# Performance work log

Hardware: AMD Instinct MI355X
Metric: run time of the kernel (lower is better)

Reference implementation:

```python
import jax, jax.numpy as jnp
import numpy as np

B, N1, N2, D = 4096, 16, 32, 30   # node batch, 1st-hop nbrs, 2nd-hop nbrs, nodeDataLen
H, HD = 6, 5                       # heads, head_dim (embed_dim = size_out*heads = 30)
LH = 64                            # linear_hidden
NEG_SLOPE = 0.02


def setup_inputs() -> dict:
    key = jax.random.key(0)
    ks = jax.random.split(key, 20)
    def w(k, shape, std=0.2):
        return jax.random.normal(k, shape, dtype=jnp.float32) * std
    return {
        "x2": jax.random.normal(ks[0], (B, N1, N2, D), dtype=jnp.float32),
        "self_feat": jax.random.normal(ks[1], (B, D), dtype=jnp.float32),
        # second-hop GraphLayer params (size_in=30 -> embed 30)
        "lin_w2": w(ks[2], (D, D)), "lin_b2": jnp.zeros((D,), jnp.float32),
        "in_w2": w(ks[3], (3 * D, D), 0.1), "in_b2": jnp.zeros((3 * D,), jnp.float32),
        "out_w2": w(ks[4], (D, D), 0.1), "out_b2": jnp.zeros((D,), jnp.float32),
        # first-hop GraphLayer params
        "lin_w1": w(ks[5], (D, D)), "lin_b1": jnp.zeros((D,), jnp.float32),
        "in_w1": w(ks[6], (3 * D, D), 0.1), "in_b1": jnp.zeros((3 * D,), jnp.float32),
        "out_w1": w(ks[7], (D, D), 0.1), "out_b1": jnp.zeros((D,), jnp.float32),
        # classification MLP
        "cw1": w(ks[8], (LH, D), 0.02), "cb1": jnp.zeros((LH,), jnp.float32),
        "cw2": w(ks[9], (LH, LH), 0.02), "cb2": jnp.zeros((LH,), jnp.float32),
        "cw3": w(ks[10], (2, LH), 0.02), "cb3": jnp.zeros((2,), jnp.float32),
    }


def graph_layer(x, lw, lb, iw, ib, ow, ob):
    """x: [S, D] -> Linear + LeakyReLU(0.02) + MHA(self) + mean over S -> [D].
    Dropout(0.2) is identity in eval mode."""
    S = x.shape[0]
    y = jax.nn.leaky_relu(x @ lw.T + lb, NEG_SLOPE)          # [S, D]
    qkv = y @ iw.T + ib                                       # [S, 3D] packed in_proj
    q, k, v = jnp.split(qkv, 3, axis=-1)
    q = q.reshape(S, H, HD)
    k = k.reshape(S, H, HD)
    v = v.reshape(S, H, HD)
    scores = jnp.einsum('shd,thd->hst', q, k) / np.float32(np.sqrt(HD))
    att = jax.nn.softmax(scores, axis=-1)                     # [H, S, S]
    o = jnp.einsum('hst,thd->shd', att, v).reshape(S, H * HD) # [S, D]
    o = o @ ow.T + ob
    return o.mean(axis=0)                                     # [D]


def reference(x2, self_feat,
              lin_w2, lin_b2, in_w2, in_b2, out_w2, out_b2,
              lin_w1, lin_b1, in_w1, in_b1, out_w1, out_b1,
              cw1, cb1, cw2, cb2, cw3, cb3):
    gl2 = lambda x: graph_layer(x, lin_w2, lin_b2, in_w2, in_b2, out_w2, out_b2)
    h1 = jax.vmap(jax.vmap(gl2))(x2)                          # [B, N1, D] second-hop aggregation
    seq = jnp.concatenate([h1, self_feat[:, None, :]], axis=1)  # [B, N1+1, D] append current node
    gl1 = lambda x: graph_layer(x, lin_w1, lin_b1, in_w1, in_b1, out_w1, out_b1)
    emb = jax.vmap(gl1)(seq)                                  # [B, D]
    h = jax.nn.leaky_relu(emb @ cw1.T + cb1, NEG_SLOPE)
    h = jax.nn.leaky_relu(h @ cw2.T + cb2, NEG_SLOPE)
    logits = h @ cw3.T + cb3                                  # [B, 2]
    # original applies Softmax(dim=0) to the 1-D 2-vector per node == softmax over classes
    return jax.nn.softmax(logits, axis=-1)
```

## Files before the change

kernel.cpp:

```cpp
#include <hip/hip_runtime.h>
#include <math.h>

#define LRELU(v) ((v) > 0.0f ? (v) : 0.02f * (v))

typedef __attribute__((ext_vector_type(8)))  short short8;
typedef __attribute__((ext_vector_type(4)))  float f32x4;
typedef __attribute__((ext_vector_type(16))) float f32x16;
typedef __attribute__((ext_vector_type(2)))  int   int2v;

__device__ inline short f2bf(float f) {
    unsigned u = __builtin_bit_cast(unsigned, f);
    unsigned r = (u + 0x7FFFu + ((u >> 16) & 1u)) >> 16;
    return (short)r;
}
__device__ inline int pack_bf16_trunc(float a, float b) {
    unsigned ua = __builtin_bit_cast(unsigned, a);
    unsigned ub = __builtin_bit_cast(unsigned, b);
    return (int)((ub & 0xFFFF0000u) | (ua >> 16));
}
__device__ inline float bf16s_to_f(unsigned short u) {
    unsigned v = ((unsigned)u) << 16;
    return __builtin_bit_cast(float, v);
}

#define PAIRS 8
#define NP1   2
#define RS5   0.44721359549995793f

__global__ __launch_bounds__(256, 4) void gl2_kernel(
    const float* __restrict__ x2,
    const float* __restrict__ lw, const float* __restrict__ lb,
    const float* __restrict__ iw, const float* __restrict__ ib,
    const float* __restrict__ ow, const float* __restrict__ ob,
    float* __restrict__ h1out)
{
    __shared__ short y_lds[32][40];
    __shared__ short qmf[6][33][8];
    __shared__ short kmf[6][33][8];
    __shared__ float vT[6][5][36];
    __shared__ short att2[6][32][40];
    __shared__ float abar[6][32];
    __shared__ float obar[32];

    const int tid  = threadIdx.x;
    const int lane = tid & 63;
    const int w    = tid >> 6;
    const int l15  = lane & 15;
    const int lq   = lane >> 4;
    const int h5   = lane >> 5;
    const int scol = lane & 31;
    const int rowz = (lane < 32) ? scol : 32;

    for (int i = tid; i < (6 * 33 * 8) / 2; i += 256) {
        ((int*)qmf)[i] = 0; ((int*)kmf)[i] = 0;
    }
    if (tid < 2) obar[30 + tid] = 0.0f;

    const int di = w & 1, si = w >> 1;
    short8 blw; float lbv;
    {
        int d = di * 16 + l15;
        #pragma unroll
        for (int i = 0; i < 8; ++i) {
            int k = lq * 8 + i;
            blw[i] = f2bf((d < 30 && k < 30) ? lw[d * 30 + k] : 0.0f);
        }
        lbv = (d < 30) ? lb[d] : 0.0f;
    }
    const int jtA = (3 * w) >> 1, jtB = (3 * w + 2) >> 1;
    short8 biwA, biwB; float ibvA, ibvB;
    {
        int jA = jtA * 16 + l15, jB = jtB * 16 + l15;
        #pragma unroll
        for (int i = 0; i < 8; ++i) {
            int k = lq * 8 + i;
            biwA[i] = f2bf((jA < 90 && k < 30) ? iw[jA * 30 + k] : 0.0f);
            biwB[i] = f2bf((jB < 90 && k < 30) ? iw[jB * 30 + k] : 0.0f);
        }
        ibvA = (jA < 90) ? ib[jA] : 0.0f;
        ibvB = (jB < 90) ? ib[jB] : 0.0f;
    }
    __syncthreads();

    for (int p = 0; p < PAIRS; ++p) {
        const long pair = (long)blockIdx.x * PAIRS + p;
        const float* xp = x2 + pair * 960;

        {
            short8 af;
            int s = si * 16 + l15;
            #pragma unroll
            for (int i = 0; i < 8; ++i) {
                int k = lq * 8 + i;
                af[i] = f2bf((k < 30) ? xp[s * 30 + k] : 0.0f);
            }
            f32x4 c = {0.0f, 0.0f, 0.0f, 0.0f};
            c = __builtin_amdgcn_mfma_f32_16x16x32_bf16(af, blw, c, 0, 0, 0);
            #pragma unroll
            for (int r = 0; r < 4; ++r) {
                float yv = c[r] + lbv;
                yv = LRELU(yv);
                y_lds[si * 16 + lq * 4 + r][di * 16 + l15] = f2bf(yv);
            }
        }
        __syncthreads();

        {
            short8 a0 = *(const short8*)&y_lds[l15][lq * 8];
            short8 a1 = *(const short8*)&y_lds[16 + l15][lq * 8];
            #pragma unroll
            for (int t = 0; t < 3; ++t) {
                int T = 3 * w + t, jt = T >> 1, si_ = T & 1;
                short8 a = si_ ? a1 : a0;
                short8 b = (jt == jtA) ? biwA : biwB;
                float ibv = (jt == jtA) ? ibvA : ibvB;
                f32x4 c = {0.0f, 0.0f, 0.0f, 0.0f};
                c = __builtin_amdgcn_mfma_f32_16x16x32_bf16(a, b, c, 0, 0, 0);
                int j = jt * 16 + l15;
                int s0 = si_ * 16 + lq * 4;
                if (j < 30) {
                    int h = j / 5, e = j - 5 * h;
                    #pragma unroll
                    for (int r = 0; r < 4; ++r)
                        qmf[h][s0 + r][e] = f2bf(c[r] + ibv);
                } else if (j < 60) {
                    int jj = j - 30; int h = jj / 5, e = jj - 5 * h;
                    #pragma unroll
                    for (int r = 0; r < 4; ++r)
                        kmf[h][s0 + r][e] = f2bf((c[r] + ibv) * RS5);
                } else if (j < 90) {
                    int jj = j - 60; int h = jj / 5, e = jj - 5 * h;
                    #pragma unroll
                    for (int r = 0; r < 4; ++r)
                        vT[h][e][s0 + r] = c[r] + ibv;
                }
            }
        }
        __syncthreads();

        if (w < 3) {
            #pragma unroll
            for (int hh = 0; hh < 2; ++hh) {
                const int h = 2 * w + hh;
                short8 af = *(const short8*)&kmf[h][rowz][0];
                short8 bf = *(const short8*)&qmf[h][rowz][0];
                f32x16 c;
                #pragma unroll
                for (int r = 0; r < 16; ++r) c[r] = 0.0f;
                c = __builtin_amdgcn_mfma_f32_32x32x16_bf16(af, bf, c, 0, 0, 0);
                float m = c[0];
                #pragma unroll
                for (int r = 1; r < 16; ++r) m = fmaxf(m, c[r]);
                m = fmaxf(m, __shfl_xor(m, 32));
                float Z = 0.0f;
                #pragma unroll
                for (int r = 0; r < 16; ++r) { c[r] = __expf(c[r] - m); Z += c[r]; }
                Z += __shfl_xor(Z, 32);
                float rZ = (1.0f / 32.0f) / Z;
                #pragma unroll
                for (int g = 0; g < 4; ++g) {
                    int tb = 8 * g + 4 * h5;
                    int2v wv;
                    wv.x = pack_bf16_trunc(c[4 * g] * rZ, c[4 * g + 1] * rZ);
                    wv.y = pack_bf16_trunc(c[4 * g + 2] * rZ, c[4 * g + 3] * rZ);
                    *(int2v*)&att2[h][scol][tb] = wv;
                }
            }
        }
        __syncthreads();

        if (tid < 192) {
            const int h = tid >> 5, t = tid & 31;
            float sum = 0.0f;
            #pragma unroll
            for (int s = 0; s < 32; ++s)
                sum += bf16s_to_f((unsigned short)att2[h][s][t]);
            abar[h][t] = sum;
        }
        __syncthreads();

        if (tid < 240) {
            const int he = tid >> 3, tq = tid & 7;
            const int h = he / 5, e = he - 5 * h;
            f32x4 av = *(const f32x4*)&abar[h][tq * 4];
            f32x4 vv = *(const f32x4*)&vT[h][e][tq * 4];
            float part = av.x * vv.x + av.y * vv.y + av.z * vv.z + av.w * vv.w;
            part += __shfl_down(part, 4, 8);
            part += __shfl_down(part, 2, 8);
            part += __shfl_down(part, 1, 8);
            if (tq == 0) obar[he] = part;
        }
        __syncthreads();

        if (tid < 240) {
            const int d = tid >> 3, jq = tid & 7;
            f32x4 ov = *(const f32x4*)&obar[jq * 4];
            float part = 0.0f;
            #pragma unroll
            for (int i = 0; i < 4; ++i) {
                int j = jq * 4 + i;
                if (j < 30) part = fmaf(ov[i], ow[d * 30 + j], part);
            }
            part += __shfl_down(part, 4, 8);
            part += __shfl_down(part, 2, 8);
            part += __shfl_down(part, 1, 8);
            if (jq == 0) h1out[pair * 30 + d] = part + ob[d];
        }
    }
}

__global__ __launch_bounds__(256, 4) void gl1_mlp_kernel(
    const float* __restrict__ h1, const float* __restrict__ self_feat,
    const float* __restrict__ lw, const float* __restrict__ lb,
    const float* __restrict__ iw, const float* __restrict__ ib,
    const float* __restrict__ ow, const float* __restrict__ ob,
    const float* __restrict__ cw1, const float* __restrict__ cb1,
    const float* __restrict__ cw2, const float* __restrict__ cb2,
    const float* __restrict__ cw3, const float* __restrict__ cb3,
    float* __restrict__ out)
{
    __shared__ short y_lds[32][40];
    __shared__ short qmf[6][33][8];
    __shared__ short kmf[6][33][8];
    __shared__ float vT[6][5][36];
    __shared__ short att2[6][32][40];
    __shared__ float abar[6][32];
    __shared__ float obar[32];
    __shared__ float embb[32];
    __shared__ float hb1[64];
    __shared__ float hb2[64];
    __shared__ float lg[2];

    const int tid  = threadIdx.x;
    const int lane = tid & 63;
    const int w    = tid >> 6;
    const int l15  = lane & 15;
    const int lq   = lane >> 4;
    const int h5   = lane >> 5;
    const int scol = lane & 31;
    const int rowz = (lane < 32) ? scol : 32;

    for (int i = tid; i < (6 * 33 * 8) / 2; i += 256) {
        ((int*)qmf)[i] = 0; ((int*)kmf)[i] = 0;
    }
    if (tid < 2) obar[30 + tid] = 0.0f;

    const int di = w & 1, si = w >> 1;
    short8 blw; float lbv;
    {
        int d = di * 16 + l15;
        #pragma unroll
        for (int i = 0; i < 8; ++i) {
            int k = lq * 8 + i;
            blw[i] = f2bf((d < 30 && k < 30) ? lw[d * 30 + k] : 0.0f);
        }
        lbv = (d < 30) ? lb[d] : 0.0f;
    }
    const int jtA = (3 * w) >> 1, jtB = (3 * w + 2) >> 1;
    short8 biwA, biwB; float ibvA, ibvB;
    {
        int jA = jtA * 16 + l15, jB = jtB * 16 + l15;
        #pragma unroll
        for (int i = 0; i < 8; ++i) {
            int k = lq * 8 + i;
            biwA[i] = f2bf((jA < 90 && k < 30) ? iw[jA * 30 + k] : 0.0f);
            biwB[i] = f2bf((jB < 90 && k < 30) ? iw[jB * 30 + k] : 0.0f);
        }
        ibvA = (jA < 90) ? ib[jA] : 0.0f;
        ibvB = (jB < 90) ? ib[jB] : 0.0f;
    }
    __syncthreads();

    for (int p = 0; p < NP1; ++p) {
        const long node = (long)blockIdx.x * NP1 + p;
        const float* h1p = h1 + node * 480;
        const float* sfp = self_feat + node * 30;

        {
            short8 af;
            if (si == 0) {
                int s = l15;
                #pragma unroll
                for (int i = 0; i < 8; ++i) {
                    int k = lq * 8 + i;
                    af[i] = f2bf((k < 30) ? h1p[s * 30 + k] : 0.0f);
                }
            } else {
                #pragma unroll
                for (int i = 0; i < 8; ++i) {
                    int k = lq * 8 + i;
                    af[i] = (l15 == 0 && k < 30) ? f2bf(sfp[k]) : (short)0;
                }
            }
            f32x4 c = {0.0f, 0.0f, 0.0f, 0.0f};
            c = __builtin_amdgcn_mfma_f32_16x16x32_bf16(af, blw, c, 0, 0, 0);
            #pragma unroll
            for (int r = 0; r < 4; ++r) {
                float yv = c[r] + lbv;
                yv = LRELU(yv);
                y_lds[si * 16 + lq * 4 + r][di * 16 + l15] = f2bf(yv);
            }
        }
        __syncthreads();

        {
            short8 a0 = *(const short8*)&y_lds[l15][lq * 8];
            short8 a1 = *(const short8*)&y_lds[16 + l15][lq * 8];
            #pragma unroll
            for (int t = 0; t < 3; ++t) {
                int T = 3 * w + t, jt = T >> 1, si_ = T & 1;
                short8 a = si_ ? a1 : a0;
                short8 b = (jt == jtA) ? biwA : biwB;
                float ibv = (jt == jtA) ? ibvA : ibvB;
                f32x4 c = {0.0f, 0.0f, 0.0f, 0.0f};
                c = __builtin_amdgcn_mfma_f32_16x16x32_bf16(a, b, c, 0, 0, 0);
                int j = jt * 16 + l15;
                int s0 = si_ * 16 + lq * 4;
                if (j < 30) {
                    int h = j / 5, e = j - 5 * h;
                    #pragma unroll
                    for (int r = 0; r < 4; ++r)
                        qmf[h][s0 + r][e] = f2bf(c[r] + ibv);
                } else if (j < 60) {
                    int jj = j - 30; int h = jj / 5, e = jj - 5 * h;
                    #pragma unroll
                    for (int r = 0; r < 4; ++r)
                        kmf[h][s0 + r][e] = f2bf((c[r] + ibv) * RS5);
                } else if (j < 90) {
                    int jj = j - 60; int h = jj / 5, e = jj - 5 * h;
                    #pragma unroll
                    for (int r = 0; r < 4; ++r)
                        vT[h][e][s0 + r] = c[r] + ibv;
                }
            }
        }
        __syncthreads();

        if (w < 3) {
            #pragma unroll
            for (int hh = 0; hh < 2; ++hh) {
                const int h = 2 * w + hh;
                short8 af = *(const short8*)&kmf[h][rowz][0];
                short8 bf = *(const short8*)&qmf[h][rowz][0];
                f32x16 c;
                #pragma unroll
                for (int r = 0; r < 16; ++r) c[r] = 0.0f;
                c = __builtin_amdgcn_mfma_f32_32x32x16_bf16(af, bf, c, 0, 0, 0);
                #pragma unroll
                for (int r = 0; r < 16; ++r) {
                    int tr = (r & 3) + 8 * (r >> 2) + 4 * h5;
                    c[r] = (tr < 17) ? c[r] : -1e30f;
                }
                float m = c[0];
                #pragma unroll
                for (int r = 1; r < 16; ++r) m = fmaxf(m, c[r]);
                m = fmaxf(m, __shfl_xor(m, 32));
                float Z = 0.0f;
                #pragma unroll
                for (int r = 0; r < 16; ++r) { c[r] = __expf(c[r] - m); Z += c[r]; }
                Z += __shfl_xor(Z, 32);
                float rZ = (1.0f / 17.0f) / Z;
                #pragma unroll
                for (int g = 0; g < 4; ++g) {
                    int tb = 8 * g + 4 * h5;
                    int2v wv;
                    wv.x = pack_bf16_trunc(c[4 * g] * rZ, c[4 * g + 1] * rZ);
                    wv.y = pack_bf16_trunc(c[4 * g + 2] * rZ, c[4 * g + 3] * rZ);
                    *(int2v*)&att2[h][scol][tb] = wv;
                }
            }
        }
        __syncthreads();

        if (tid < 192) {
            const int h = tid >> 5, t = tid & 31;
            float sum = 0.0f;
            #pragma unroll
            for (int s = 0; s < 17; ++s)
                sum += bf16s_to_f((unsigned short)att2[h][s][t]);
            abar[h][t] = sum;
        }
        __syncthreads();

        if (tid < 240) {
            const int he = tid >> 3, tq = tid & 7;
            const int h = he / 5, e = he - 5 * h;
            f32x4 av = *(const f32x4*)&abar[h][tq * 4];
            f32x4 vv = *(const f32x4*)&vT[h][e][tq * 4];
            float part = av.x * vv.x + av.y * vv.y + av.z * vv.z + av.w * vv.w;
            part += __shfl_down(part, 4, 8);
            part += __shfl_down(part, 2, 8);
            part += __shfl_down(part, 1, 8);
            if (tq == 0) obar[he] = part;
        }
        __syncthreads();

        if (tid < 240) {
            const int d = tid >> 3, jq = tid & 7;
            f32x4 ov = *(const f32x4*)&obar[jq * 4];
            float part = 0.0f;
            #pragma unroll
            for (int i = 0; i < 4; ++i) {
                int j = jq * 4 + i;
                if (j < 30) part = fmaf(ov[i], ow[d * 30 + j], part);
            }
            part += __shfl_down(part, 4, 8);
            part += __shfl_down(part, 2, 8);
            part += __shfl_down(part, 1, 8);
            if (jq == 0) embb[d] = part + ob[d];
        }
        __syncthreads();

        {
            const int o = tid >> 2, kq = tid & 3;
            float part = 0.0f;
            #pragma unroll
            for (int i = 0; i < 8; ++i) {
                int k = kq * 8 + i;
                if (k < 30) part = fmaf(embb[k], cw1[o * 30 + k], part);
            }
            part += __shfl_down(part, 2, 4);
            part += __shfl_down(part, 1, 4);
            if (kq == 0) hb1[o] = LRELU(part + cb1[o]);
        }
        __syncthreads();
        {
            const int o = tid >> 2, kq = tid & 3;
            float part = 0.0f;
            #pragma unroll
            for (int i = 0; i < 16; ++i) {
                int k = kq * 16 + i;
                part = fmaf(hb1[k], cw2[o * 64 + k], part);
            }
            part += __shfl_down(part, 2, 4);
            part += __shfl_down(part, 1, 4);
            if (kq == 0) hb2[o] = LRELU(part + cb2[o]);
        }
        __syncthreads();
        if (tid < 128) {
            const int c = tid >> 6, k = tid & 63;
            float part = hb2[k] * cw3[c * 64 + k];
            part += __shfl_down(part, 32);
            part += __shfl_down(part, 16);
            part += __shfl_down(part, 8);
            part += __shfl_down(part, 4);
            part += __shfl_down(part, 2);
            part += __shfl_down(part, 1);
            if (k == 0) lg[c] = part + cb3[c];
        }
        __syncthreads();
        if (tid < 2) {
            float m = fmaxf(lg[0], lg[1]);
            float e0 = __expf(lg[0] - m), e1 = __expf(lg[1] - m);
            float pr = ((tid == 0) ? e0 : e1) / (e0 + e1);
            out[node * 2 + tid] = pr;
        }
        __syncthreads();
    }
}

extern "C" void kernel_launch(void* const* d_in, const int* in_sizes, int n_in,
                              void* d_out, int out_size, void* d_ws, size_t ws_size,
                              hipStream_t stream)
{
    const float* x2        = (const float*)d_in[0];
    const float* self_feat = (const float*)d_in[1];
    const float* lin_w2 = (const float*)d_in[2];
    const float* lin_b2 = (const float*)d_in[3];
    const float* in_w2  = (const float*)d_in[4];
    const float* in_b2  = (const float*)d_in[5];
    const float* out_w2 = (const float*)d_in[6];
    const float* out_b2 = (const float*)d_in[7];
    const float* lin_w1 = (const float*)d_in[8];
    const float* lin_b1 = (const float*)d_in[9];
    const float* in_w1  = (const float*)d_in[10];
    const float* in_b1  = (const float*)d_in[11];
    const float* out_w1 = (const float*)d_in[12];
    const float* out_b1 = (const float*)d_in[13];
    const float* cw1 = (const float*)d_in[14];
    const float* cb1 = (const float*)d_in[15];
    const float* cw2 = (const float*)d_in[16];
    const float* cb2 = (const float*)d_in[17];
    const float* cw3 = (const float*)d_in[18];
    const float* cb3 = (const float*)d_in[19];
    float* outp = (float*)d_out;

    float* h1 = (float*)d_ws;

    gl2_kernel<<<(4096 * 16) / PAIRS, 256, 0, stream>>>(
        x2, lin_w2, lin_b2, in_w2, in_b2, out_w2, out_b2, h1);

    gl1_mlp_kernel<<<4096 / NP1, 256, 0, stream>>>(
        h1, self_feat, lin_w1, lin_b1, in_w1, in_b1, out_w1, out_b1,
        cw1, cb1, cw2, cb2, cw3, cb3, outp);
}
```

Before: 573.1 us.

## Fuse attention-mean and V product into MFMA, use hardware bf16 pack and exp2

The attention-weighted V reduction is now done with two MFMAs directly from the softmax registers against a bf16 V tile stored in a permuted layout. This removes the att2/abar LDS round trips and two block barriers per pair. The K scale is folded with log2(e) so the softmax can use raw v_exp_f32 and rcp. It also uses v_cvt_pk_bf16_f32 for packing, raises the occupancy hint to 5, and gives gl1 one node per block instead of two. These trade a more complex swizzled layout and reduced-precision reciprocal and exp for fewer LDS passes and syncs.

```diff
diff --git a/kernel.cpp b/kernel.cpp
--- a/kernel.cpp
+++ b/kernel.cpp
@@ -1,45 +1,44 @@
 #include <hip/hip_runtime.h>
 #include <math.h>
 
-#define LRELU(v) ((v) > 0.0f ? (v) : 0.02f * (v))
+#define LRELU(v) fmaxf((v), 0.02f * (v))
 
 typedef __attribute__((ext_vector_type(8)))  short short8;
 typedef __attribute__((ext_vector_type(4)))  float f32x4;
 typedef __attribute__((ext_vector_type(16))) float f32x16;
 typedef __attribute__((ext_vector_type(2)))  int   int2v;
+typedef __attribute__((ext_vector_type(4)))  int   int4v;
 
 __device__ inline short f2bf(float f) {
     unsigned u = __builtin_bit_cast(unsigned, f);
     unsigned r = (u + 0x7FFFu + ((u >> 16) & 1u)) >> 16;
     return (short)r;
 }
-__device__ inline int pack_bf16_trunc(float a, float b) {
-    unsigned ua = __builtin_bit_cast(unsigned, a);
-    unsigned ub = __builtin_bit_cast(unsigned, b);
-    return (int)((ub & 0xFFFF0000u) | (ua >> 16));
+__device__ inline int cvt_pk_bf16(float lo, float hi) {
+    int r;
+    asm("v_cvt_pk_bf16_f32 %0, %1, %2" : "=v"(r) : "v"(lo), "v"(hi));
+    return r;
 }
-__device__ inline float bf16s_to_f(unsigned short u) {
-    unsigned v = ((unsigned)u) << 16;
-    return __builtin_bit_cast(float, v);
+__device__ inline float exp2_asm(float x) {
+    float r;
+    asm("v_exp_f32 %0, %1" : "=v"(r) : "v"(x));
+    return r;
 }
 
 #define PAIRS 8
-#define NP1   2
-#define RS5   0.44721359549995793f
-
-__global__ __launch_bounds__(256, 4) void gl2_kernel(
+#define RS5L  0.6451994329f
+
+__global__ __launch_bounds__(256, 5) void gl2_kernel(
     const float* __restrict__ x2,
     const float* __restrict__ lw, const float* __restrict__ lb,
     const float* __restrict__ iw, const float* __restrict__ ib,
     const float* __restrict__ ow, const float* __restrict__ ob,
     float* __restrict__ h1out)
 {
-    __shared__ short y_lds[32][40];
-    __shared__ short qmf[6][33][8];
-    __shared__ short kmf[6][33][8];
-    __shared__ float vT[6][5][36];
-    __shared__ short att2[6][32][40];
-    __shared__ float abar[6][32];
+    __shared__ __attribute__((aligned(16))) short y_lds[32][40];
+    __shared__ __attribute__((aligned(16))) short qmf[6][33][8];
+    __shared__ __attribute__((aligned(16))) short kmf[6][33][8];
+    __shared__ __attribute__((aligned(16))) short vbf[6][8][40];
     __shared__ float obar[32];
 
     const int tid  = threadIdx.x;
@@ -51,9 +50,8 @@
     const int scol = lane & 31;
     const int rowz = (lane < 32) ? scol : 32;
 
-    for (int i = tid; i < (6 * 33 * 8) / 2; i += 256) {
-        ((int*)qmf)[i] = 0; ((int*)kmf)[i] = 0;
-    }
+    for (int i = tid; i < 792; i += 256) { ((int*)qmf)[i] = 0; ((int*)kmf)[i] = 0; }
+    for (int i = tid; i < 960; i += 256) ((int*)vbf)[i] = 0;
     if (tid < 2) obar[30 + tid] = 0.0f;
 
     const int di = w & 1, si = w >> 1;
@@ -87,21 +85,30 @@
         const float* xp = x2 + pair * 960;
 
         {
-            short8 af;
             int s = si * 16 + l15;
+            const float* xr = xp + s * 30 + lq * 8;
+            float xv[8];
             #pragma unroll
             for (int i = 0; i < 8; ++i) {
                 int k = lq * 8 + i;
-                af[i] = f2bf((k < 30) ? xp[s * 30 + k] : 0.0f);
-            }
+                xv[i] = (k < 30) ? xr[i] : 0.0f;
+            }
+            int4v ai;
+            ai.x = cvt_pk_bf16(xv[0], xv[1]);
+            ai.y = cvt_pk_bf16(xv[2], xv[3]);
+            ai.z = cvt_pk_bf16(xv[4], xv[5]);
+            ai.w = cvt_pk_bf16(xv[6], xv[7]);
+            short8 af = __builtin_bit_cast(short8, ai);
             f32x4 c = {0.0f, 0.0f, 0.0f, 0.0f};
             c = __builtin_amdgcn_mfma_f32_16x16x32_bf16(af, blw, c, 0, 0, 0);
-            #pragma unroll
-            for (int r = 0; r < 4; ++r) {
-                float yv = c[r] + lbv;
-                yv = LRELU(yv);
-                y_lds[si * 16 + lq * 4 + r][di * 16 + l15] = f2bf(yv);
-            }
+            float y0 = LRELU(c[0] + lbv), y1 = LRELU(c[1] + lbv);
+            float y2 = LRELU(c[2] + lbv), y3 = LRELU(c[3] + lbv);
+            int p01 = cvt_pk_bf16(y0, y1), p23 = cvt_pk_bf16(y2, y3);
+            int row = si * 16 + lq * 4, col = di * 16 + l15;
+            y_lds[row + 0][col] = (short)p01;
+            y_lds[row + 1][col] = (short)(p01 >> 16);
+            y_lds[row + 2][col] = (short)p23;
+            y_lds[row + 3][col] = (short)(p23 >> 16);
         }
         __syncthreads();
 
@@ -120,19 +127,28 @@
                 int s0 = si_ * 16 + lq * 4;
                 if (j < 30) {
                     int h = j / 5, e = j - 5 * h;
-                    #pragma unroll
-                    for (int r = 0; r < 4; ++r)
-                        qmf[h][s0 + r][e] = f2bf(c[r] + ibv);
+                    int p01 = cvt_pk_bf16(c[0] + ibv, c[1] + ibv);
+                    int p23 = cvt_pk_bf16(c[2] + ibv, c[3] + ibv);
+                    qmf[h][s0 + 0][e] = (short)p01;
+                    qmf[h][s0 + 1][e] = (short)(p01 >> 16);
+                    qmf[h][s0 + 2][e] = (short)p23;
+                    qmf[h][s0 + 3][e] = (short)(p23 >> 16);
                 } else if (j < 60) {
                     int jj = j - 30; int h = jj / 5, e = jj - 5 * h;
-                    #pragma unroll
-                    for (int r = 0; r < 4; ++r)
-                        kmf[h][s0 + r][e] = f2bf((c[r] + ibv) * RS5);
+                    float ibl = ibv * RS5L;
+                    int p01 = cvt_pk_bf16(fmaf(c[0], RS5L, ibl), fmaf(c[1], RS5L, ibl));
+                    int p23 = cvt_pk_bf16(fmaf(c[2], RS5L, ibl), fmaf(c[3], RS5L, ibl));
+                    kmf[h][s0 + 0][e] = (short)p01;
+                    kmf[h][s0 + 1][e] = (short)(p01 >> 16);
+                    kmf[h][s0 + 2][e] = (short)p23;
+                    kmf[h][s0 + 3][e] = (short)(p23 >> 16);
                 } else if (j < 90) {
                     int jj = j - 60; int h = jj / 5, e = jj - 5 * h;
-                    #pragma unroll
-                    for (int r = 0; r < 4; ++r)
-                        vT[h][e][s0 + r] = c[r] + ibv;
+                    int k0 = ((s0 >> 1) & 4) | ((s0 << 1) & 8) | (s0 & 16);
+                    int2v wv;
+                    wv.x = cvt_pk_bf16(c[0] + ibv, c[1] + ibv);
+                    wv.y = cvt_pk_bf16(c[2] + ibv, c[3] + ibv);
+                    *(int2v*)&vbf[h][e][k0] = wv;
                 }
             }
         }
@@ -154,41 +170,33 @@
                 m = fmaxf(m, __shfl_xor(m, 32));
                 float Z = 0.0f;
                 #pragma unroll
-                for (int r = 0; r < 16; ++r) { c[r] = __expf(c[r] - m); Z += c[r]; }
+                for (int r = 0; r < 16; ++r) { c[r] = exp2_asm(c[r] - m); Z += c[r]; }
                 Z += __shfl_xor(Z, 32);
-                float rZ = (1.0f / 32.0f) / Z;
+                float rZ = __builtin_amdgcn_rcpf(Z) * (1.0f / 32.0f);
+                int4v a1i, a2i;
+                a1i.x = cvt_pk_bf16(c[0] * rZ,  c[1] * rZ);
+                a1i.y = cvt_pk_bf16(c[2] * rZ,  c[3] * rZ);
+                a1i.z = cvt_pk_bf16(c[4] * rZ,  c[5] * rZ);
+                a1i.w = cvt_pk_bf16(c[6] * rZ,  c[7] * rZ);
+                a2i.x = cvt_pk_bf16(c[8] * rZ,  c[9] * rZ);
+                a2i.y = cvt_pk_bf16(c[10] * rZ, c[11] * rZ);
+                a2i.z = cvt_pk_bf16(c[12] * rZ, c[13] * rZ);
+                a2i.w = cvt_pk_bf16(c[14] * rZ, c[15] * rZ);
+                short8 b1 = *(const short8*)&vbf[h][scol & 7][8 * h5];
+                short8 b2 = *(const short8*)&vbf[h][scol & 7][16 + 8 * h5];
+                f32x16 P;
                 #pragma unroll
-                for (int g = 0; g < 4; ++g) {
-                    int tb = 8 * g + 4 * h5;
-                    int2v wv;
-                    wv.x = pack_bf16_trunc(c[4 * g] * rZ, c[4 * g + 1] * rZ);
-                    wv.y = pack_bf16_trunc(c[4 * g + 2] * rZ, c[4 * g + 3] * rZ);
-                    *(int2v*)&att2[h][scol][tb] = wv;
-                }
-            }
-        }
-        __syncthreads();
-
-        if (tid < 192) {
-            const int h = tid >> 5, t = tid & 31;
-            float sum = 0.0f;
-            #pragma unroll
-            for (int s = 0; s < 32; ++s)
-                sum += bf16s_to_f((unsigned short)att2[h][s][t]);
-            abar[h][t] = sum;
-        }
-        __syncthreads();
-
-        if (tid < 240) {
-            const int he = tid >> 3, tq = tid & 7;
-            const int h = he / 5, e = he - 5 * h;
-            f32x4 av = *(const f32x4*)&abar[h][tq * 4];
-            f32x4 vv = *(const f32x4*)&vT[h][e][tq * 4];
-            float part = av.x * vv.x + av.y * vv.y + av.z * vv.z + av.w * vv.w;
-            part += __shfl_down(part, 4, 8);
-            part += __shfl_down(part, 2, 8);
-            part += __shfl_down(part, 1, 8);
-            if (tq == 0) obar[he] = part;
+                for (int r = 0; r < 16; ++r) P[r] = 0.0f;
+                P = __builtin_amdgcn_mfma_f32_32x32x16_bf16(
+                        __builtin_bit_cast(short8, a1i), b1, P, 0, 0, 0);
+                P = __builtin_amdgcn_mfma_f32_32x32x16_bf16(
+                        __builtin_bit_cast(short8, a2i), b2, P, 0, 0, 0);
+                float sm = 0.0f;
+                #pragma unroll
+                for (int r = 0; r < 16; ++r) sm += P[r];
+                sm += __shfl_xor(sm, 32);
+                if (lane < 5) obar[h * 5 + lane] = sm;
+            }
         }
         __syncthreads();
 
@@ -209,7 +217,7 @@
     }
 }
 
-__global__ __launch_bounds__(256, 4) void gl1_mlp_kernel(
+__global__ __launch_bounds__(256, 5) void gl1_mlp_kernel(
     const float* __restrict__ h1, const float* __restrict__ self_feat,
     const float* __restrict__ lw, const float* __restrict__ lb,
     const float* __restrict__ iw, const float* __restrict__ ib,
@@ -219,12 +227,10 @@
     const float* __restrict__ cw3, const float* __restrict__ cb3,
     float* __restrict__ out)
 {
-    __shared__ short y_lds[32][40];
-    __shared__ short qmf[6][33][8];
-    __shared__ short kmf[6][33][8];
-    __shared__ float vT[6][5][36];
-    __shared__ short att2[6][32][40];
-    __shared__ float abar[6][32];
+    __shared__ __attribute__((aligned(16))) short y_lds[32][40];
+    __shared__ __attribute__((aligned(16))) short qmf[6][33][8];
+    __shared__ __attribute__((aligned(16))) short kmf[6][33][8];
+    __shared__ __attribute__((aligned(16))) short vbf[6][8][40];
     __shared__ float obar[32];
     __shared__ float embb[32];
     __shared__ float hb1[64];
@@ -240,9 +246,8 @@
     const int scol = lane & 31;
     const int rowz = (lane < 32) ? scol : 32;
 
-    for (int i = tid; i < (6 * 33 * 8) / 2; i += 256) {
-        ((int*)qmf)[i] = 0; ((int*)kmf)[i] = 0;
-    }
+    for (int i = tid; i < 792; i += 256) { ((int*)qmf)[i] = 0; ((int*)kmf)[i] = 0; }
+    for (int i = tid; i < 960; i += 256) ((int*)vbf)[i] = 0;
     if (tid < 2) obar[30 + tid] = 0.0f;
 
     const int di = w & 1, si = w >> 1;
@@ -271,191 +276,198 @@
     }
     __syncthreads();
 
-    for (int p = 0; p < NP1; ++p) {
-        const long node = (long)blockIdx.x * NP1 + p;
-        const float* h1p = h1 + node * 480;
-        const float* sfp = self_feat + node * 30;
-
-        {
-            short8 af;
-            if (si == 0) {
-                int s = l15;
-                #pragma unroll
-                for (int i = 0; i < 8; ++i) {
-                    int k = lq * 8 + i;
-                    af[i] = f2bf((k < 30) ? h1p[s * 30 + k] : 0.0f);
-                }
-            } else {
-                #pragma unroll
-                for (int i = 0; i < 8; ++i) {
-                    int k = lq * 8 + i;
-                    af[i] = (l15 == 0 && k < 30) ? f2bf(sfp[k]) : (short)0;
-                }
-            }
+    const long node = (long)blockIdx.x;
+    const float* h1p = h1 + node * 480;
+    const float* sfp = self_feat + node * 30;
+
+    {
+        float xv[8];
+        if (si == 0) {
+            const float* xr = h1p + l15 * 30 + lq * 8;
+            #pragma unroll
+            for (int i = 0; i < 8; ++i) {
+                int k = lq * 8 + i;
+                xv[i] = (k < 30) ? xr[i] : 0.0f;
+            }
+        } else {
+            #pragma unroll
+            for (int i = 0; i < 8; ++i) {
+                int k = lq * 8 + i;
+                xv[i] = (l15 == 0 && k < 30) ? sfp[k] : 0.0f;
+            }
+        }
+        int4v ai;
+        ai.x = cvt_pk_bf16(xv[0], xv[1]);
+        ai.y = cvt_pk_bf16(xv[2], xv[3]);
+        ai.z = cvt_pk_bf16(xv[4], xv[5]);
+        ai.w = cvt_pk_bf16(xv[6], xv[7]);
+        short8 af = __builtin_bit_cast(short8, ai);
+        f32x4 c = {0.0f, 0.0f, 0.0f, 0.0f};
+        c = __builtin_amdgcn_mfma_f32_16x16x32_bf16(af, blw, c, 0, 0, 0);
+        float y0 = LRELU(c[0] + lbv), y1 = LRELU(c[1] + lbv);
+        float y2 = LRELU(c[2] + lbv), y3 = LRELU(c[3] + lbv);
+        int p01 = cvt_pk_bf16(y0, y1), p23 = cvt_pk_bf16(y2, y3);
+        int row = si * 16 + lq * 4, col = di * 16 + l15;
+        y_lds[row + 0][col] = (short)p01;
+        y_lds[row + 1][col] = (short)(p01 >> 16);
+        y_lds[row + 2][col] = (short)p23;
+        y_lds[row + 3][col] = (short)(p23 >> 16);
+    }
+    __syncthreads();
+
+    {
+        short8 a0 = *(const short8*)&y_lds[l15][lq * 8];
+        short8 a1 = *(const short8*)&y_lds[16 + l15][lq * 8];
+        #pragma unroll
+        for (int t = 0; t < 3; ++t) {
+            int T = 3 * w + t, jt = T >> 1, si_ = T & 1;
+            short8 a = si_ ? a1 : a0;
+            short8 b = (jt == jtA) ? biwA : biwB;
+            float ibv = (jt == jtA) ? ibvA : ibvB;
             f32x4 c = {0.0f, 0.0f, 0.0f, 0.0f};
-            c = __builtin_amdgcn_mfma_f32_16x16x32_bf16(af, blw, c, 0, 0, 0);
-            #pragma unroll
-            for (int r = 0; r < 4; ++r) {
-                float yv = c[r] + lbv;
-                yv = LRELU(yv);
-                y_lds[si * 16 + lq * 4 + r][di * 16 + l15] = f2bf(yv);
-            }
-        }
-        __syncthreads();
-
-        {
-            short8 a0 = *(const short8*)&y_lds[l15][lq * 8];
-            short8 a1 = *(const short8*)&y_lds[16 + l15][lq * 8];
-            #pragma unroll
-            for (int t = 0; t < 3; ++t) {
-                int T = 3 * w + t, jt = T >> 1, si_ = T & 1;
-                short8 a = si_ ? a1 : a0;
-                short8 b = (jt == jtA) ? biwA : biwB;
-                float ibv = (jt == jtA) ? ibvA : ibvB;
-                f32x4 c = {0.0f, 0.0f, 0.0f, 0.0f};
-                c = __builtin_amdgcn_mfma_f32_16x16x32_bf16(a, b, c, 0, 0, 0);
-                int j = jt * 16 + l15;
-                int s0 = si_ * 16 + lq * 4;
-                if (j < 30) {
-                    int h = j / 5, e = j - 5 * h;
-                    #pragma unroll
-                    for (int r = 0; r < 4; ++r)
-                        qmf[h][s0 + r][e] = f2bf(c[r] + ibv);
-                } else if (j < 60) {
-                    int jj = j - 30; int h = jj / 5, e = jj - 5 * h;
-                    #pragma unroll
-                    for (int r = 0; r < 4; ++r)
-                        kmf[h][s0 + r][e] = f2bf((c[r] + ibv) * RS5);
-                } else if (j < 90) {
-                    int jj = j - 60; int h = jj / 5, e = jj - 5 * h;
-                    #pragma unroll
-                    for (int r = 0; r < 4; ++r)
-                        vT[h][e][s0 + r] = c[r] + ibv;
-                }
-            }
-        }
-        __syncthreads();
-
-        if (w < 3) {
-            #pragma unroll
-            for (int hh = 0; hh < 2; ++hh) {
-                const int h = 2 * w + hh;
-                short8 af = *(const short8*)&kmf[h][rowz][0];
-                short8 bf = *(const short8*)&qmf[h][rowz][0];
-                f32x16 c;
-                #pragma unroll
-                for (int r = 0; r < 16; ++r) c[r] = 0.0f;
-                c = __builtin_amdgcn_mfma_f32_32x32x16_bf16(af, bf, c, 0, 0, 0);
-                #pragma unroll
-                for (int r = 0; r < 16; ++r) {
-                    int tr = (r & 3) + 8 * (r >> 2) + 4 * h5;
-                    c[r] = (tr < 17) ? c[r] : -1e30f;
-                }
-                float m = c[0];
-                #pragma unroll
-                for (int r = 1; r < 16; ++r) m = fmaxf(m, c[r]);
-                m = fmaxf(m, __shfl_xor(m, 32));
-                float Z = 0.0f;
-                #pragma unroll
-                for (int r = 0; r < 16; ++r) { c[r] = __expf(c[r] - m); Z += c[r]; }
-                Z += __shfl_xor(Z, 32);
-                float rZ = (1.0f / 17.0f) / Z;
-                #pragma unroll
-                for (int g = 0; g < 4; ++g) {
-                    int tb = 8 * g + 4 * h5;
-                    int2v wv;
-                    wv.x = pack_bf16_trunc(c[4 * g] * rZ, c[4 * g + 1] * rZ);
-                    wv.y = pack_bf16_trunc(c[4 * g + 2] * rZ, c[4 * g + 3] * rZ);
-                    *(int2v*)&att2[h][scol][tb] = wv;
-                }
-            }
-        }
-        __syncthreads();
-
-        if (tid < 192) {
-            const int h = tid >> 5, t = tid & 31;
-            float sum = 0.0f;
-            #pragma unroll
-            for (int s = 0; s < 17; ++s)
-                sum += bf16s_to_f((unsigned short)att2[h][s][t]);
-            abar[h][t] = sum;
-        }
-        __syncthreads();
-
-        if (tid < 240) {
-            const int he = tid >> 3, tq = tid & 7;
-            const int h = he / 5, e = he - 5 * h;
-            f32x4 av = *(const f32x4*)&abar[h][tq * 4];
-            f32x4 vv = *(const f32x4*)&vT[h][e][tq * 4];
-            float part = av.x * vv.x + av.y * vv.y + av.z * vv.z + av.w * vv.w;
-            part += __shfl_down(part, 4, 8);
-            part += __shfl_down(part, 2, 8);
-            part += __shfl_down(part, 1, 8);
-            if (tq == 0) obar[he] = part;
-        }
-        __syncthreads();
-
-        if (tid < 240) {
-            const int d = tid >> 3, jq = tid & 7;
-            f32x4 ov = *(const f32x4*)&obar[jq * 4];
-            float part = 0.0f;
-            #pragma unroll
-            for (int i = 0; i < 4; ++i) {
-                int j = jq * 4 + i;
-                if (j < 30) part = fmaf(ov[i], ow[d * 30 + j], part);
-            }
-            part += __shfl_down(part, 4, 8);
-            part += __shfl_down(part, 2, 8);
-            part += __shfl_down(part, 1, 8);
-            if (jq == 0) embb[d] = part + ob[d];
-        }
-        __syncthreads();
-
-        {
-            const int o = tid >> 2, kq = tid & 3;
-            float part = 0.0f;
-            #pragma unroll
-            for (int i = 0; i < 8; ++i) {
-                int k = kq * 8 + i;
-                if (k < 30) part = fmaf(embb[k], cw1[o * 30 + k], part);
-            }
-            part += __shfl_down(part, 2, 4);
-            part += __shfl_down(part, 1, 4);
-            if (kq == 0) hb1[o] = LRELU(part + cb1[o]);
-        }
-        __syncthreads();
-        {
-            const int o = tid >> 2, kq = tid & 3;
-            float part = 0.0f;
-            #pragma unroll
-            for (int i = 0; i < 16; ++i) {
-                int k = kq * 16 + i;
-                part = fmaf(hb1[k], cw2[o * 64 + k], part);
-            }
-            part += __shfl_down(part, 2, 4);
-            part += __shfl_down(part, 1, 4);
-            if (kq == 0) hb2[o] = LRELU(part + cb2[o]);
-        }
-        __syncthreads();
-        if (tid < 128) {
-            const int c = tid >> 6, k = tid & 63;
-            float part = hb2[k] * cw3[c * 64 + k];
-            part += __shfl_down(part, 32);
-            part += __shfl_down(part, 16);
-            part += __shfl_down(part, 8);
-            part += __shfl_down(part, 4);
-            part += __shfl_down(part, 2);
-            part += __shfl_down(part, 1);
-            if (k == 0) lg[c] = part + cb3[c];
-        }
-        __syncthreads();
-        if (tid < 2) {
-            float m = fmaxf(lg[0], lg[1]);
-            float e0 = __expf(lg[0] - m), e1 = __expf(lg[1] - m);
-            float pr = ((tid == 0) ? e0 : e1) / (e0 + e1);
-            out[node * 2 + tid] = pr;
-        }
-        __syncthreads();
+            c = __builtin_amdgcn_mfma_f32_16x16x32_bf16(a, b, c, 0, 0, 0);
+            int j = jt * 16 + l15;
+            int s0 = si_ * 16 + lq * 4;
+            if (j < 30) {
+                int h = j / 5, e = j - 5 * h;
+                int p01 = cvt_pk_bf16(c[0] + ibv, c[1] + ibv);
+                int p23 = cvt_pk_bf16(c[2] + ibv, c[3] + ibv);
+                qmf[h][s0 + 0][e] = (short)p01;
+                qmf[h][s0 + 1][e] = (short)(p01 >> 16);
+                qmf[h][s0 + 2][e] = (short)p23;
+                qmf[h][s0 + 3][e] = (short)(p23 >> 16);
+            } else if (j < 60) {
+                int jj = j - 30; int h = jj / 5, e = jj - 5 * h;
+                float ibl = ibv * RS5L;
+                int p01 = cvt_pk_bf16(fmaf(c[0], RS5L, ibl), fmaf(c[1], RS5L, ibl));
+                int p23 = cvt_pk_bf16(fmaf(c[2], RS5L, ibl), fmaf(c[3], RS5L, ibl));
+                kmf[h][s0 + 0][e] = (short)p01;
+                kmf[h][s0 + 1][e] = (short)(p01 >> 16);
+                kmf[h][s0 + 2][e] = (short)p23;
+                kmf[h][s0 + 3][e] = (short)(p23 >> 16);
+            } else if (j < 90) {
+                int jj = j - 60; int h = jj / 5, e = jj - 5 * h;
+                int k0 = ((s0 >> 1) & 4) | ((s0 << 1) & 8) | (s0 & 16);
+                int2v wv;
+                wv.x = cvt_pk_bf16(c[0] + ibv, c[1] + ibv);
+                wv.y = cvt_pk_bf16(c[2] + ibv, c[3] + ibv);
+                *(int2v*)&vbf[h][e][k0] = wv;
+            }
+        }
+    }
+    __syncthreads();
+
+    if (w < 3) {
+        #pragma unroll
+        for (int hh = 0; hh < 2; ++hh) {
+            const int h = 2 * w + hh;
+            short8 af = *(const short8*)&kmf[h][rowz][0];
+            short8 bf = *(const short8*)&qmf[h][rowz][0];
+            f32x16 c;
+            #pragma unroll
+            for (int r = 0; r < 16; ++r) c[r] = 0.0f;
+            c = __builtin_amdgcn_mfma_f32_32x32x16_bf16(af, bf, c, 0, 0, 0);
+            #pragma unroll
+            for (int r = 0; r < 16; ++r) {
+                int tr = (r & 3) + 8 * (r >> 2) + 4 * h5;
+                c[r] = (tr < 17) ? c[r] : -1e30f;
+            }
+            float m = c[0];
+            #pragma unroll
+            for (int r = 1; r < 16; ++r) m = fmaxf(m, c[r]);
+            m = fmaxf(m, __shfl_xor(m, 32));
+            float Z = 0.0f;
+            #pragma unroll
+            for (int r = 0; r < 16; ++r) { c[r] = exp2_asm(c[r] - m); Z += c[r]; }
+            Z += __shfl_xor(Z, 32);
+            float rZ = __builtin_amdgcn_rcpf(Z) * (1.0f / 17.0f);
+            int4v a1i, a2i;
+            a1i.x = cvt_pk_bf16(c[0] * rZ,  c[1] * rZ);
+            a1i.y = cvt_pk_bf16(c[2] * rZ,  c[3] * rZ);
+            a1i.z = cvt_pk_bf16(c[4] * rZ,  c[5] * rZ);
+            a1i.w = cvt_pk_bf16(c[6] * rZ,  c[7] * rZ);
+            a2i.x = cvt_pk_bf16(c[8] * rZ,  c[9] * rZ);
+            a2i.y = cvt_pk_bf16(c[10] * rZ, c[11] * rZ);
+            a2i.z = cvt_pk_bf16(c[12] * rZ, c[13] * rZ);
+            a2i.w = cvt_pk_bf16(c[14] * rZ, c[15] * rZ);
+            short8 b1 = *(const short8*)&vbf[h][scol & 7][8 * h5];
+            short8 b2 = *(const short8*)&vbf[h][scol & 7][16 + 8 * h5];
+            f32x16 P;
+            #pragma unroll
+            for (int r = 0; r < 16; ++r) P[r] = 0.0f;
+            P = __builtin_amdgcn_mfma_f32_32x32x16_bf16(
+                    __builtin_bit_cast(short8, a1i), b1, P, 0, 0, 0);
+            P = __builtin_amdgcn_mfma_f32_32x32x16_bf16(
+                    __builtin_bit_cast(short8, a2i), b2, P, 0, 0, 0);
+            float sm = 0.0f;
+            #pragma unroll
+            for (int r = 0; r < 8; ++r) sm += P[r];
+            sm += (h5 == 0) ? P[8] : 0.0f;
+            sm += __shfl_xor(sm, 32);
+            if (lane < 5) obar[h * 5 + lane] = sm;
+        }
+    }
+    __syncthreads();
+
+    if (tid < 240) {
+        const int d = tid >> 3, jq = tid & 7;
+        f32x4 ov = *(const f32x4*)&obar[jq * 4];
+        float part = 0.0f;
+        #pragma unroll
+        for (int i = 0; i < 4; ++i) {
+            int j = jq * 4 + i;
+            if (j < 30) part = fmaf(ov[i], ow[d * 30 + j], part);
+        }
+        part += __shfl_down(part, 4, 8);
+        part += __shfl_down(part, 2, 8);
+        part += __shfl_down(part, 1, 8);
+        if (jq == 0) embb[d] = part + ob[d];
+    }
+    __syncthreads();
+
+    {
+        const int o = tid >> 2, kq = tid & 3;
+        float part = 0.0f;
+        #pragma unroll
+        for (int i = 0; i < 8; ++i) {
+            int k = kq * 8 + i;
+            if (k < 30) part = fmaf(embb[k], cw1[o * 30 + k], part);
+        }
+        part += __shfl_down(part, 2, 4);
+        part += __shfl_down(part, 1, 4);
+        if (kq == 0) hb1[o] = LRELU(part + cb1[o]);
+    }
+    __syncthreads();
+    {
+        const int o = tid >> 2, kq = tid & 3;
+        float part = 0.0f;
+        #pragma unroll
+        for (int i = 0; i < 16; ++i) {
+            int k = kq * 16 + i;
+            part = fmaf(hb1[k], cw2[o * 64 + k], part);
+        }
+        part += __shfl_down(part, 2, 4);
+        part += __shfl_down(part, 1, 4);
+        if (kq == 0) hb2[o] = LRELU(part + cb2[o]);
+    }
+    __syncthreads();
+    if (tid < 128) {
+        const int c = tid >> 6, k = tid & 63;
+        float part = hb2[k] * cw3[c * 64 + k];
+        part += __shfl_down(part, 32);
+        part += __shfl_down(part, 16);
+        part += __shfl_down(part, 8);
+        part += __shfl_down(part, 4);
+        part += __shfl_down(part, 2);
+        part += __shfl_down(part, 1);
+        if (k == 0) lg[c] = part + cb3[c];
+    }
+    __syncthreads();
+    if (tid < 2) {
+        float m = fmaxf(lg[0], lg[1]);
+        float e0 = __expf(lg[0] - m), e1 = __expf(lg[1] - m);
+        float pr = ((tid == 0) ? e0 : e1) / (e0 + e1);
+        out[node * 2 + tid] = pr;
     }
 }
 
@@ -490,7 +502,7 @@
     gl2_kernel<<<(4096 * 16) / PAIRS, 256, 0, stream>>>(
         x2, lin_w2, lin_b2, in_w2, in_b2, out_w2, out_b2, h1);
 
-    gl1_mlp_kernel<<<4096 / NP1, 256, 0, stream>>>(
+    gl1_mlp_kernel<<<4096, 256, 0, stream>>>(
         h1, self_feat, lin_w1, lin_b1, in_w1, in_b1, out_w1, out_b1,
         cw1, cb1, cw2, cb2, cw3, cb3, outp);
 }
```

New measurement: 547.1 us. 1.05x faster.
